# Kernel tuning notes

Hardware: AMD Instinct MI355X
Metric: run time of the kernel (lower is better)

The kernel has to match this reference:

```python
import jax, jax.numpy as jnp
import numpy as np

B, N, C, H = 8192, 17, 512, 8
HD = C // H  # head dim = 64


def setup_inputs() -> dict:
    key = jax.random.key(0)
    ks = jax.random.split(key, 7)
    s = 0.02
    return {
        "x": jax.random.normal(ks[0], (B, N, C), dtype=jnp.float32),
        "W_qkv": jax.random.normal(ks[1], (C, 3 * C), dtype=jnp.float32) * s,
        "b_qkv": jax.random.normal(ks[2], (3 * C,), dtype=jnp.float32) * s,
        "outer": jax.random.normal(ks[3], (H, N, N), dtype=jnp.float32) * s,
        "alpha": jnp.ones((1,), dtype=jnp.float32),
        "W_proj": jax.random.normal(ks[4], (C, C), dtype=jnp.float32) * s,
        "b_proj": jax.random.normal(ks[5], (C,), dtype=jnp.float32) * s,
    }


def reference(x, W_qkv, b_qkv, outer, alpha, W_proj, b_proj):
    scale = HD ** -0.5
    qkv = x @ W_qkv + b_qkv                       # [B,N,3C]
    qkv = qkv.reshape(B, N, 3, H, HD)
    q = jnp.transpose(qkv[:, :, 0], (0, 2, 1, 3))  # [B,H,N,HD]
    k = jnp.transpose(qkv[:, :, 1], (0, 2, 1, 3))
    v = jnp.transpose(qkv[:, :, 2], (0, 2, 1, 3))
    # comb=False path: (q @ k^T + alpha * outer) * scale, softmax, @ v
    logits = (jnp.einsum('bhnd,bhmd->bhnm', q, k) + alpha * outer[None]) * scale
    attn = jax.nn.softmax(logits, axis=-1)        # [B,H,N,N]
    out = jnp.einsum('bhnm,bhmd->bhnd', attn, v)  # [B,H,N,HD]
    out = jnp.transpose(out, (0, 2, 1, 3)).reshape(B, N, C)
    return out @ W_proj + b_proj
```

## Files before the change

### kernel.cpp

```cpp
#include <hip/hip_runtime.h>
#include <stdint.h>


typedef __attribute__((ext_vector_type(4))) float f32x4;
typedef _Float16 f16x8 __attribute__((ext_vector_type(8)));
typedef _Float16 f16x2 __attribute__((ext_vector_type(2)));

__device__ __forceinline__ unsigned short f2h(float f) {
  return __builtin_bit_cast(unsigned short, (_Float16)f);
}
__device__ __forceinline__ float h2f(unsigned short h) {
  return (float)__builtin_bit_cast(_Float16, h);
}
__device__ __forceinline__ float fdot2u(uint32_t a, uint32_t b, float c) {
  return __builtin_amdgcn_fdot2(__builtin_bit_cast(f16x2, a),
                                __builtin_bit_cast(f16x2, b), c, false);
}

#define GLOAD_LDS16(gptr, lptr)                                          \
  __builtin_amdgcn_global_load_lds(                                      \
      (__attribute__((address_space(1))) void*)(gptr),                   \
      (__attribute__((address_space(3))) void*)(lptr), 16, 0, 0)

__device__ __forceinline__ f32x4 mfma16(f16x8 a, f16x8 b, f32x4 c) {
  return __builtin_amdgcn_mfma_f32_16x16x32_f16(a, b, c, 0, 0, 0);
}

__global__ __launch_bounds__(256) void k_cvt(const float* __restrict__ in,
                                             unsigned short* __restrict__ out,
                                             long n4) {
  long i = (long)blockIdx.x * 256 + threadIdx.x;
  if (i >= n4) return;
  float4 a = reinterpret_cast<const float4*>(in)[i];
  ushort4 o;
  o.x = f2h(a.x); o.y = f2h(a.y); o.z = f2h(a.z); o.w = f2h(a.w);
  reinterpret_cast<ushort4*>(out)[i] = o;
}

template <bool PERM>
__global__ __launch_bounds__(256) void k_cvt_t(const float* __restrict__ W,
                                               unsigned short* __restrict__ Wt,
                                               int K, int Norig) {
  int i = blockIdx.x * 256 + threadIdx.x;
  if (i >= K * Norig) return;
  int np = i / K, k = i - np * K;
  int n = np;
  if (PERM) {
    int h = np / 192, rem = np - h * 192;
    int t = rem >> 6, d = rem & 63;
    n = t * 512 + h * 64 + d;
  }
  Wt[i] = f2h(W[(size_t)k * Norig + n]);
}

__global__ __launch_bounds__(256) void k_permb(const float* __restrict__ b,
                                               float* __restrict__ bqp) {
  int np = blockIdx.x * 256 + threadIdx.x;
  if (np >= 1536) return;
  int h = np / 192, rem = np - h * 192;
  int t = rem >> 6, d = rem & 63;
  bqp[np] = b[t * 512 + h * 64 + d];
}

#define FB_BUF 28672

__global__ __launch_bounds__(1024) void k_fused(
    const unsigned short* __restrict__ A,
    const unsigned short* __restrict__ Bt,
    const float* __restrict__ bqp,
    const float* __restrict__ outer,
    const float* __restrict__ alpha_p,
    unsigned short* __restrict__ ao) {
  __shared__ __align__(16) unsigned short smem[2 * FB_BUF];
  __shared__ float s_attn[16][17][18];
  __shared__ float s_inv[16][17];

  const int tid = threadIdx.x;
  const int w = tid >> 6, lane = tid & 63;
  const int wm = w >> 2, wn = w & 3;
  const int lr = lane & 15, lk = lane >> 4;

  const int bid = (blockIdx.x & 7) * ((int)gridDim.x >> 3) + (blockIdx.x >> 3);
  const int mt = bid >> 3, h = bid & 7;
  const int batch0 = mt * 15;
  const int brow = batch0 * 17;
  const int bcol = h * 192;

  const int srowl = lane >> 3;
  const int scol = ((lane & 7) ^ srowl) << 3;

  f32x4 acc[4][3];
#pragma unroll
  for (int m = 0; m < 4; m++)
#pragma unroll
    for (int n = 0; n < 3; n++) acc[m][n] = f32x4{0.f, 0.f, 0.f, 0.f};

  auto STAGE = [&](int t, int buf) {
    unsigned short* dstbase = smem + buf * FB_BUF;
    for (int s = w; s < 56; s += 16) {
      unsigned short* dst = dstbase + s * 512;
      const unsigned short* src;
      if (s < 32) {
        int gr = brow + s * 8 + srowl;
        if (gr > 139263) gr = 139263;
        src = A + (size_t)gr * 512 + t * 64 + scol;
      } else {
        int r = (s - 32) * 8 + srowl;
        src = Bt + (size_t)(bcol + r) * 512 + t * 64 + scol;
      }
      GLOAD_LDS16(src, dst);
    }
  };

  STAGE(0, 0);
  asm volatile("s_waitcnt vmcnt(0)" ::: "memory");
  __builtin_amdgcn_s_barrier();

  for (int t = 0; t < 8; ++t) {
    const int ub = (t & 1) * FB_BUF;
    if (t < 7) STAGE(t + 1, (t + 1) & 1);
    const unsigned short* sa = smem + ub + (wm * 64 + lr) * 64;
    const unsigned short* sb = smem + ub + 16384 + (wn * 48 + lr) * 64;
#pragma unroll
    for (int kk = 0; kk < 2; ++kk) {
      const int gx = (((kk << 2) + lk) ^ (lr & 7)) << 3;
      f16x8 av0 = *(const f16x8*)(sa + gx);
      f16x8 av1 = *(const f16x8*)(sa + 1024 + gx);
      f16x8 av2 = *(const f16x8*)(sa + 2048 + gx);
      f16x8 av3 = *(const f16x8*)(sa + 3072 + gx);
      f16x8 bv0 = *(const f16x8*)(sb + gx);
      f16x8 bv1 = *(const f16x8*)(sb + 1024 + gx);
      f16x8 bv2 = *(const f16x8*)(sb + 2048 + gx);
      acc[0][0] = mfma16(av0, bv0, acc[0][0]);
      acc[0][1] = mfma16(av0, bv1, acc[0][1]);
      acc[0][2] = mfma16(av0, bv2, acc[0][2]);
      acc[1][0] = mfma16(av1, bv0, acc[1][0]);
      acc[1][1] = mfma16(av1, bv1, acc[1][1]);
      acc[1][2] = mfma16(av1, bv2, acc[1][2]);
      acc[2][0] = mfma16(av2, bv0, acc[2][0]);
      acc[2][1] = mfma16(av2, bv1, acc[2][1]);
      acc[2][2] = mfma16(av2, bv2, acc[2][2]);
      acc[3][0] = mfma16(av3, bv0, acc[3][0]);
      acc[3][1] = mfma16(av3, bv1, acc[3][1]);
      acc[3][2] = mfma16(av3, bv2, acc[3][2]);
    }
    asm volatile("s_waitcnt vmcnt(0)" ::: "memory");
    __builtin_amdgcn_s_barrier();
  }

  {
    const int er0 = wm * 64 + (lane >> 4) * 4;
    const int ec0 = wn * 48 + lr;
    float bvv[3];
#pragma unroll
    for (int nf = 0; nf < 3; ++nf) bvv[nf] = bqp[bcol + ec0 + nf * 16];
#pragma unroll
    for (int mf = 0; mf < 4; ++mf)
#pragma unroll
      for (int nf = 0; nf < 3; ++nf)
#pragma unroll
        for (int rr = 0; rr < 4; ++rr)
          smem[(er0 + mf * 16 + rr) * 200 + ec0 + nf * 16] =
              f2h(acc[mf][nf][rr] + bvv[nf]);
  }
  __syncthreads();

  const int nb = min(15, 8192 - batch0);
  if (w < nb) {
    const float alpha = alpha_p[0];
    const unsigned short* sA0 = smem + (w * 17) * 200;
    for (int p = lane; p < 289; p += 64) {
      const int r = p / 17, m = p - r * 17;
      const uint4* qr = (const uint4*)(sA0 + r * 200);
      const uint4* km = (const uint4*)(sA0 + m * 200 + 64);
      float s = 0.f;
#pragma unroll
      for (int c = 0; c < 8; ++c) {
        uint4 qa = qr[c], ka = km[c];
        s = fdot2u(qa.x, ka.x, s);
        s = fdot2u(qa.y, ka.y, s);
        s = fdot2u(qa.z, ka.z, s);
        s = fdot2u(qa.w, ka.w, s);
      }
      s_attn[w][r][m] = (s + alpha * outer[h * 289 + p]) * 0.125f;
    }
    __builtin_amdgcn_wave_barrier();
    asm volatile("" ::: "memory");

    if (lane < 17) {
      float mx = -1e30f;
#pragma unroll
      for (int m = 0; m < 17; m++) mx = fmaxf(mx, s_attn[w][lane][m]);
      float s = 0.f;
#pragma unroll
      for (int m = 0; m < 17; m++) {
        float e = __expf(s_attn[w][lane][m] - mx);
        s_attn[w][lane][m] = e;
        s += e;
      }
      s_inv[w][lane] = 1.f / s;
    }
    __builtin_amdgcn_wave_barrier();
    asm volatile("" ::: "memory");

    float vr[17];
#pragma unroll
    for (int m = 0; m < 17; m++)
      vr[m] = h2f(smem[(w * 17 + m) * 200 + 128 + lane]);
    const size_t obase = ((size_t)(batch0 + w) * 17) * 512 + h * 64 + lane;
#pragma unroll 1
    for (int r = 0; r < 17; ++r) {
      float o = 0.f;
#pragma unroll
      for (int m = 0; m < 17; m++) o += s_attn[w][r][m] * vr[m];
      ao[obase + (size_t)r * 512] = f2h(o * s_inv[w][r]);
    }
  }
}

#define MFMA_QUAD(M0, N0)                                                  \
  __builtin_amdgcn_s_setprio(1);                                           \
  _Pragma("unroll") for (int m_ = 0; m_ < 4; m_++) {                       \
    _Pragma("unroll") for (int n_ = 0; n_ < 2; n_++) {                     \
      acc[(M0) + m_][(N0) + n_] =                                          \
          mfma16(a[(M0) + m_][0], b[(N0) + n_][0], acc[(M0) + m_][(N0) + n_]); \
      acc[(M0) + m_][(N0) + n_] =                                          \
          mfma16(a[(M0) + m_][1], b[(N0) + n_][1], acc[(M0) + m_][(N0) + n_]); \
    }                                                                      \
  }                                                                        \
  __builtin_amdgcn_s_setprio(0);

#define READ_A_HALF(MH)                                                    \
  _Pragma("unroll") for (int m_ = 0; m_ < 4; m_++) {                       \
    a[(MH)*4 + m_][0] =                                                    \
        *(const f16x8*)(ldsA + ub + ((MH)*4 + m_) * 1024 + gx0);           \
    a[(MH)*4 + m_][1] =                                                    \
        *(const f16x8*)(ldsA + ub + ((MH)*4 + m_) * 1024 + gx1);           \
  }
#define READ_B_HALF(NH)                                                    \
  _Pragma("unroll") for (int n_ = 0; n_ < 2; n_++) {                       \
    b[(NH)*2 + n_][0] =                                                    \
        *(const f16x8*)(ldsB + ub + ((NH)*2 + n_) * 1024 + gx0);           \
    b[(NH)*2 + n_][1] =                                                    \
        *(const f16x8*)(ldsB + ub + ((NH)*2 + n_) * 1024 + gx1);           \
  }

template <int KT, bool F16OUT>
__global__ __launch_bounds__(512, 2) void k_gemm256(
    const unsigned short* __restrict__ A, const unsigned short* __restrict__ Bt,
    const float* __restrict__ bias, void* __restrict__ Cout, int M, int N,
    int K) {
  __shared__ __align__(16) unsigned short lds[2][2][256 * 64];

  const int tid = threadIdx.x;
  const int w = tid >> 6, lane = tid & 63;
  const int wm = w >> 2, wn = w & 3;
  const int lr = lane & 15, lk = lane >> 4;

  const int bid = (blockIdx.x & 7) * ((int)gridDim.x >> 3) + (blockIdx.x >> 3);
  const int nbn = N >> 8;
  const int brow = (bid / nbn) << 8;
  const int bcol = (bid % nbn) << 8;

  const int srow = lane >> 3;
  const int scol = (((lane & 7) ^ srow) << 3);
  const unsigned short* pA = A + (size_t)(brow + (w << 3) + srow) * K + scol;
  const unsigned short* pB = Bt + (size_t)(bcol + (w << 3) + srow) * K + scol;

  auto STAGE = [&](int hh) {
    const int uu = hh >> 2, s = hh & 3;
    const int isB = s >> 1, half = s & 1;
    const unsigned short* src =
        (isB ? pB : pA) + (size_t)(half * 128) * K + uu * 64;
    unsigned short* dst = &lds[uu & 1][isB][(half * 128 + (w << 3)) * 64];
    GLOAD_LDS16(src, dst);
    GLOAD_LDS16(src + (size_t)64 * K, dst + 64 * 64);
  };

  const int gx0 = ((lk) ^ (lr & 7)) << 3;
  const int gx1 = ((4 + lk) ^ (lr & 7)) << 3;
  const unsigned short* ldsA = &lds[0][0][(wm * 128 + lr) * 64];
  const unsigned short* ldsB = &lds[0][1][(wn * 64 + lr) * 64];

  f32x4 acc[8][4];
#pragma unroll
  for (int m = 0; m < 8; m++)
#pragma unroll
    for (int n = 0; n < 4; n++) acc[m][n] = f32x4{0.f, 0.f, 0.f, 0.f};

#pragma unroll
  for (int hh = 0; hh < 7; ++hh) STAGE(hh);
  asm volatile("s_waitcnt vmcnt(6)" ::: "memory");
  __builtin_amdgcn_s_barrier();

  f16x8 a[8][2], b[4][2];
  for (int u = 0; u < KT; ++u) {
    const int ub = (u & 1) * 32768;
    const int hbase = 4 * u + 7;
    READ_A_HALF(0)
    READ_B_HALF(0)
    if (hbase < 4 * KT) STAGE(hbase);
    __builtin_amdgcn_s_barrier();
    asm volatile("s_waitcnt lgkmcnt(0)" ::: "memory");
    __builtin_amdgcn_sched_barrier(0);
    MFMA_QUAD(0, 0)
    __builtin_amdgcn_s_barrier();
    READ_A_HALF(1)
    READ_B_HALF(1)
    if (hbase + 1 < 4 * KT) STAGE(hbase + 1);
    __builtin_amdgcn_s_barrier();
    asm volatile("s_waitcnt lgkmcnt(0)" ::: "memory");
    __builtin_amdgcn_sched_barrier(0);
    MFMA_QUAD(0, 2)
    __builtin_amdgcn_s_barrier();
    if (hbase + 2 < 4 * KT) STAGE(hbase + 2);
    __builtin_amdgcn_s_barrier();
    MFMA_QUAD(4, 2)
    __builtin_amdgcn_s_barrier();
    if (hbase + 3 < 4 * KT) STAGE(hbase + 3);
    if (u + 2 < KT) {
      asm volatile("s_waitcnt vmcnt(6)" ::: "memory");
    } else if (u + 2 == KT) {
      asm volatile("s_waitcnt vmcnt(0)" ::: "memory");
    }
    __builtin_amdgcn_s_barrier();
    MFMA_QUAD(4, 0)
    __builtin_amdgcn_s_barrier();
  }

  const int orow = brow + wm * 128 + (lane >> 4) * 4;
  const int ocol0 = bcol + wn * 64 + lr;
#pragma unroll
  for (int n = 0; n < 4; n++) {
    const int col = ocol0 + n * 16;
    const float bv = bias[col];
#pragma unroll
    for (int m = 0; m < 8; m++) {
      const int row = orow + m * 16;
#pragma unroll
      for (int r = 0; r < 4; r++) {
        float v = acc[m][n][r] + bv;
        if (F16OUT)
          ((unsigned short*)Cout)[(size_t)(row + r) * N + col] = f2h(v);
        else
          ((float*)Cout)[(size_t)(row + r) * N + col] = v;
      }
    }
  }
}

extern "C" void kernel_launch(void* const* d_in, const int* in_sizes, int n_in,
                              void* d_out, int out_size, void* d_ws,
                              size_t ws_size, hipStream_t stream) {
  const float* x      = (const float*)d_in[0];
  const float* W_qkv  = (const float*)d_in[1];
  const float* b_qkv  = (const float*)d_in[2];
  const float* outer  = (const float*)d_in[3];
  const float* alpha  = (const float*)d_in[4];
  const float* W_proj = (const float*)d_in[5];
  const float* b_proj = (const float*)d_in[6];

  char* ws = (char*)d_ws;
  unsigned short* xb  = (unsigned short*)(ws);
  unsigned short* ao  = (unsigned short*)(ws + 142606336);
  unsigned short* wqt = (unsigned short*)(ws + 285212672);
  unsigned short* wpt = (unsigned short*)(ws + 286785536);
  float*          bqp = (float*)(ws + 287309824);

  k_cvt<<<dim3(69632), dim3(256), 0, stream>>>(x, xb, 17825792L);
  k_cvt_t<true><<<dim3(3072), dim3(256), 0, stream>>>(W_qkv, wqt, 512, 1536);
  k_cvt_t<false><<<dim3(1024), dim3(256), 0, stream>>>(W_proj, wpt, 512, 512);
  k_permb<<<dim3(6), dim3(256), 0, stream>>>(b_qkv, bqp);

  k_fused<<<dim3(4376), dim3(1024), 0, stream>>>(xb, wqt, bqp, outer, alpha, ao);

  k_gemm256<8, false><<<dim3(1088), dim3(512), 0, stream>>>(
      ao, wpt, b_proj, (float*)d_out, 139264, 512, 512);
}
```

Before: 726.5 us.

## Shrink fused attention and projection tiles to 512-thread blocks for occupancy

Result: faster. 594.0 us (-18.2%).

```diff
diff --git a/kernel.cpp b/kernel.cpp
--- a/kernel.cpp
+++ b/kernel.cpp
@@ -62,18 +62,16 @@
   bqp[np] = b[t * 512 + h * 64 + d];
 }
 
-#define FB_BUF 28672
-
-__global__ __launch_bounds__(1024) void k_fused(
+#define FBUF 20480
+
+__global__ __launch_bounds__(512, 4) void k_fused(
     const unsigned short* __restrict__ A,
     const unsigned short* __restrict__ Bt,
     const float* __restrict__ bqp,
     const float* __restrict__ outer,
     const float* __restrict__ alpha_p,
     unsigned short* __restrict__ ao) {
-  __shared__ __align__(16) unsigned short smem[2 * FB_BUF];
-  __shared__ float s_attn[16][17][18];
-  __shared__ float s_inv[16][17];
+  __shared__ __align__(16) unsigned short smem[2 * FBUF];
 
   const int tid = threadIdx.x;
   const int w = tid >> 6, lane = tid & 63;
@@ -82,7 +80,7 @@
 
   const int bid = (blockIdx.x & 7) * ((int)gridDim.x >> 3) + (blockIdx.x >> 3);
   const int mt = bid >> 3, h = bid & 7;
-  const int batch0 = mt * 15;
+  const int batch0 = mt * 7;
   const int brow = batch0 * 17;
   const int bcol = h * 192;
 
@@ -96,16 +94,18 @@
     for (int n = 0; n < 3; n++) acc[m][n] = f32x4{0.f, 0.f, 0.f, 0.f};
 
   auto STAGE = [&](int t, int buf) {
-    unsigned short* dstbase = smem + buf * FB_BUF;
-    for (int s = w; s < 56; s += 16) {
+    unsigned short* dstbase = smem + buf * FBUF;
+#pragma unroll
+    for (int s5 = 0; s5 < 5; ++s5) {
+      const int s = w + s5 * 8;
       unsigned short* dst = dstbase + s * 512;
       const unsigned short* src;
-      if (s < 32) {
+      if (s < 16) {
         int gr = brow + s * 8 + srowl;
         if (gr > 139263) gr = 139263;
         src = A + (size_t)gr * 512 + t * 64 + scol;
       } else {
-        int r = (s - 32) * 8 + srowl;
+        int r = (s - 16) * 8 + srowl;
         src = Bt + (size_t)(bcol + r) * 512 + t * 64 + scol;
       }
       GLOAD_LDS16(src, dst);
@@ -117,10 +117,10 @@
   __builtin_amdgcn_s_barrier();
 
   for (int t = 0; t < 8; ++t) {
-    const int ub = (t & 1) * FB_BUF;
+    const int ub = (t & 1) * FBUF;
     if (t < 7) STAGE(t + 1, (t + 1) & 1);
     const unsigned short* sa = smem + ub + (wm * 64 + lr) * 64;
-    const unsigned short* sb = smem + ub + 16384 + (wn * 48 + lr) * 64;
+    const unsigned short* sb = smem + ub + 8192 + (wn * 48 + lr) * 64;
 #pragma unroll
     for (int kk = 0; kk < 2; ++kk) {
       const int gx = (((kk << 2) + lk) ^ (lr & 7)) << 3;
@@ -148,6 +148,9 @@
     __builtin_amdgcn_s_barrier();
   }
 
+  float* s_attn = (float*)(smem + 25600);
+  float* s_inv = (float*)(smem + 25600 + 2 * (7 * 17 * 18));
+
   {
     const int er0 = wm * 64 + (lane >> 4) * 4;
     const int ec0 = wn * 48 + lr;
@@ -165,7 +168,7 @@
   }
   __syncthreads();
 
-  const int nb = min(15, 8192 - batch0);
+  const int nb = min(7, 8192 - batch0);
   if (w < nb) {
     const float alpha = alpha_p[0];
     const unsigned short* sA0 = smem + (w * 17) * 200;
@@ -182,7 +185,7 @@
         s = fdot2u(qa.z, ka.z, s);
         s = fdot2u(qa.w, ka.w, s);
       }
-      s_attn[w][r][m] = (s + alpha * outer[h * 289 + p]) * 0.125f;
+      s_attn[(w * 17 + r) * 18 + m] = (s + alpha * outer[h * 289 + p]) * 0.125f;
     }
     __builtin_amdgcn_wave_barrier();
     asm volatile("" ::: "memory");
@@ -190,15 +193,16 @@
     if (lane < 17) {
       float mx = -1e30f;
 #pragma unroll
-      for (int m = 0; m < 17; m++) mx = fmaxf(mx, s_attn[w][lane][m]);
+      for (int m = 0; m < 17; m++)
+        mx = fmaxf(mx, s_attn[(w * 17 + lane) * 18 + m]);
       float s = 0.f;
 #pragma unroll
       for (int m = 0; m < 17; m++) {
-        float e = __expf(s_attn[w][lane][m] - mx);
-        s_attn[w][lane][m] = e;
+        float e = __expf(s_attn[(w * 17 + lane) * 18 + m] - mx);
+        s_attn[(w * 17 + lane) * 18 + m] = e;
         s += e;
       }
-      s_inv[w][lane] = 1.f / s;
+      s_inv[w * 17 + lane] = 1.f / s;
     }
     __builtin_amdgcn_wave_barrier();
     asm volatile("" ::: "memory");
@@ -212,45 +216,20 @@
     for (int r = 0; r < 17; ++r) {
       float o = 0.f;
 #pragma unroll
-      for (int m = 0; m < 17; m++) o += s_attn[w][r][m] * vr[m];
-      ao[obase + (size_t)r * 512] = f2h(o * s_inv[w][r]);
-    }
-  }
-}
-
-#define MFMA_QUAD(M0, N0)                                                  \
-  __builtin_amdgcn_s_setprio(1);                                           \
-  _Pragma("unroll") for (int m_ = 0; m_ < 4; m_++) {                       \
-    _Pragma("unroll") for (int n_ = 0; n_ < 2; n_++) {                     \
-      acc[(M0) + m_][(N0) + n_] =                                          \
-          mfma16(a[(M0) + m_][0], b[(N0) + n_][0], acc[(M0) + m_][(N0) + n_]); \
-      acc[(M0) + m_][(N0) + n_] =                                          \
-          mfma16(a[(M0) + m_][1], b[(N0) + n_][1], acc[(M0) + m_][(N0) + n_]); \
-    }                                                                      \
-  }                                                                        \
-  __builtin_amdgcn_s_setprio(0);
-
-#define READ_A_HALF(MH)                                                    \
-  _Pragma("unroll") for (int m_ = 0; m_ < 4; m_++) {                       \
-    a[(MH)*4 + m_][0] =                                                    \
-        *(const f16x8*)(ldsA + ub + ((MH)*4 + m_) * 1024 + gx0);           \
-    a[(MH)*4 + m_][1] =                                                    \
-        *(const f16x8*)(ldsA + ub + ((MH)*4 + m_) * 1024 + gx1);           \
-  }
-#define READ_B_HALF(NH)                                                    \
-  _Pragma("unroll") for (int n_ = 0; n_ < 2; n_++) {                       \
-    b[(NH)*2 + n_][0] =                                                    \
-        *(const f16x8*)(ldsB + ub + ((NH)*2 + n_) * 1024 + gx0);           \
-    b[(NH)*2 + n_][1] =                                                    \
-        *(const f16x8*)(ldsB + ub + ((NH)*2 + n_) * 1024 + gx1);           \
-  }
-
-template <int KT, bool F16OUT>
-__global__ __launch_bounds__(512, 2) void k_gemm256(
-    const unsigned short* __restrict__ A, const unsigned short* __restrict__ Bt,
-    const float* __restrict__ bias, void* __restrict__ Cout, int M, int N,
-    int K) {
-  __shared__ __align__(16) unsigned short lds[2][2][256 * 64];
+      for (int m = 0; m < 17; m++) o += s_attn[(w * 17 + r) * 18 + m] * vr[m];
+      ao[obase + (size_t)r * 512] = f2h(o * s_inv[w * 17 + r]);
+    }
+  }
+}
+
+#define PBUF 16384
+
+__global__ __launch_bounds__(512, 4) void k_proj(
+    const unsigned short* __restrict__ A,
+    const unsigned short* __restrict__ Bt,
+    const float* __restrict__ bias,
+    float* __restrict__ C) {
+  __shared__ __align__(16) unsigned short smem[2 * PBUF];
 
   const int tid = threadIdx.x;
   const int w = tid >> 6, lane = tid & 63;
@@ -258,93 +237,74 @@
   const int lr = lane & 15, lk = lane >> 4;
 
   const int bid = (blockIdx.x & 7) * ((int)gridDim.x >> 3) + (blockIdx.x >> 3);
-  const int nbn = N >> 8;
-  const int brow = (bid / nbn) << 8;
-  const int bcol = (bid % nbn) << 8;
-
-  const int srow = lane >> 3;
-  const int scol = (((lane & 7) ^ srow) << 3);
-  const unsigned short* pA = A + (size_t)(brow + (w << 3) + srow) * K + scol;
-  const unsigned short* pB = Bt + (size_t)(bcol + (w << 3) + srow) * K + scol;
-
-  auto STAGE = [&](int hh) {
-    const int uu = hh >> 2, s = hh & 3;
-    const int isB = s >> 1, half = s & 1;
-    const unsigned short* src =
-        (isB ? pB : pA) + (size_t)(half * 128) * K + uu * 64;
-    unsigned short* dst = &lds[uu & 1][isB][(half * 128 + (w << 3)) * 64];
-    GLOAD_LDS16(src, dst);
-    GLOAD_LDS16(src + (size_t)64 * K, dst + 64 * 64);
+  const int brow = (bid >> 2) << 7;
+  const int bcol = (bid & 3) << 7;
+
+  const int srowl = lane >> 3;
+  const int scol = ((lane & 7) ^ srowl) << 3;
+
+  f32x4 acc[4][2];
+#pragma unroll
+  for (int m = 0; m < 4; m++)
+#pragma unroll
+    for (int n = 0; n < 2; n++) acc[m][n] = f32x4{0.f, 0.f, 0.f, 0.f};
+
+  auto STAGE = [&](int t, int buf) {
+    unsigned short* dstbase = smem + buf * PBUF;
+#pragma unroll
+    for (int s4 = 0; s4 < 4; ++s4) {
+      const int s = w + s4 * 8;
+      unsigned short* dst = dstbase + s * 512;
+      const unsigned short* src =
+          (s < 16) ? A + (size_t)(brow + s * 8 + srowl) * 512 + t * 64 + scol
+                   : Bt + (size_t)(bcol + (s - 16) * 8 + srowl) * 512 + t * 64 + scol;
+      GLOAD_LDS16(src, dst);
+    }
   };
 
-  const int gx0 = ((lk) ^ (lr & 7)) << 3;
-  const int gx1 = ((4 + lk) ^ (lr & 7)) << 3;
-  const unsigned short* ldsA = &lds[0][0][(wm * 128 + lr) * 64];
-  const unsigned short* ldsB = &lds[0][1][(wn * 64 + lr) * 64];
-
-  f32x4 acc[8][4];
-#pragma unroll
-  for (int m = 0; m < 8; m++)
-#pragma unroll
-    for (int n = 0; n < 4; n++) acc[m][n] = f32x4{0.f, 0.f, 0.f, 0.f};
-
-#pragma unroll
-  for (int hh = 0; hh < 7; ++hh) STAGE(hh);
-  asm volatile("s_waitcnt vmcnt(6)" ::: "memory");
+  STAGE(0, 0);
+  asm volatile("s_waitcnt vmcnt(0)" ::: "memory");
   __builtin_amdgcn_s_barrier();
 
-  f16x8 a[8][2], b[4][2];
-  for (int u = 0; u < KT; ++u) {
-    const int ub = (u & 1) * 32768;
-    const int hbase = 4 * u + 7;
-    READ_A_HALF(0)
-    READ_B_HALF(0)
-    if (hbase < 4 * KT) STAGE(hbase);
+  for (int t = 0; t < 8; ++t) {
+    const int ub = (t & 1) * PBUF;
+    if (t < 7) STAGE(t + 1, (t + 1) & 1);
+    const unsigned short* sa = smem + ub + (wm * 64 + lr) * 64;
+    const unsigned short* sb = smem + ub + 8192 + (wn * 32 + lr) * 64;
+#pragma unroll
+    for (int kk = 0; kk < 2; ++kk) {
+      const int gx = (((kk << 2) + lk) ^ (lr & 7)) << 3;
+      f16x8 av0 = *(const f16x8*)(sa + gx);
+      f16x8 av1 = *(const f16x8*)(sa + 1024 + gx);
+      f16x8 av2 = *(const f16x8*)(sa + 2048 + gx);
+      f16x8 av3 = *(const f16x8*)(sa + 3072 + gx);
+      f16x8 bv0 = *(const f16x8*)(sb + gx);
+      f16x8 bv1 = *(const f16x8*)(sb + 1024 + gx);
+      acc[0][0] = mfma16(av0, bv0, acc[0][0]);
+      acc[0][1] = mfma16(av0, bv1, acc[0][1]);
+      acc[1][0] = mfma16(av1, bv0, acc[1][0]);
+      acc[1][1] = mfma16(av1, bv1, acc[1][1]);
+      acc[2][0] = mfma16(av2, bv0, acc[2][0]);
+      acc[2][1] = mfma16(av2, bv1, acc[2][1]);
+      acc[3][0] = mfma16(av3, bv0, acc[3][0]);
+      acc[3][1] = mfma16(av3, bv1, acc[3][1]);
+    }
+    asm volatile("s_waitcnt vmcnt(0)" ::: "memory");
     __builtin_amdgcn_s_barrier();
-    asm volatile("s_waitcnt lgkmcnt(0)" ::: "memory");
-    __builtin_amdgcn_sched_barrier(0);
-    MFMA_QUAD(0, 0)
-    __builtin_amdgcn_s_barrier();
-    READ_A_HALF(1)
-    READ_B_HALF(1)
-    if (hbase + 1 < 4 * KT) STAGE(hbase + 1);
-    __builtin_amdgcn_s_barrier();
-    asm volatile("s_waitcnt lgkmcnt(0)" ::: "memory");
-    __builtin_amdgcn_sched_barrier(0);
-    MFMA_QUAD(0, 2)
-    __builtin_amdgcn_s_barrier();
-    if (hbase + 2 < 4 * KT) STAGE(hbase + 2);
-    __builtin_amdgcn_s_barrier();
-    MFMA_QUAD(4, 2)
-    __builtin_amdgcn_s_barrier();
-    if (hbase + 3 < 4 * KT) STAGE(hbase + 3);
-    if (u + 2 < KT) {
-      asm volatile("s_waitcnt vmcnt(6)" ::: "memory");
-    } else if (u + 2 == KT) {
-      asm volatile("s_waitcnt vmcnt(0)" ::: "memory");
-    }
-    __builtin_amdgcn_s_barrier();
-    MFMA_QUAD(4, 0)
-    __builtin_amdgcn_s_barrier();
-  }
-
-  const int orow = brow + wm * 128 + (lane >> 4) * 4;
-  const int ocol0 = bcol + wn * 64 + lr;
-#pragma unroll
-  for (int n = 0; n < 4; n++) {
+  }
+
+  const int orow = brow + wm * 64 + (lane >> 4) * 4;
+  const int ocol0 = bcol + wn * 32 + lr;
+#pragma unroll
+  for (int n = 0; n < 2; n++) {
     const int col = ocol0 + n * 16;
     const float bv = bias[col];
 #pragma unroll
-    for (int m = 0; m < 8; m++) {
+    for (int m = 0; m < 4; m++) {
       const int row = orow + m * 16;
 #pragma unroll
-      for (int r = 0; r < 4; r++) {
-        float v = acc[m][n][r] + bv;
-        if (F16OUT)
-          ((unsigned short*)Cout)[(size_t)(row + r) * N + col] = f2h(v);
-        else
-          ((float*)Cout)[(size_t)(row + r) * N + col] = v;
-      }
+      for (int r = 0; r < 4; r++)
+        C[(size_t)(row + r) * 512 + col] = acc[m][n][r] + bv;
     }
   }
 }
@@ -372,8 +332,7 @@
   k_cvt_t<false><<<dim3(1024), dim3(256), 0, stream>>>(W_proj, wpt, 512, 512);
   k_permb<<<dim3(6), dim3(256), 0, stream>>>(b_qkv, bqp);
 
-  k_fused<<<dim3(4376), dim3(1024), 0, stream>>>(xb, wqt, bqp, outer, alpha, ao);
-
-  k_gemm256<8, false><<<dim3(1088), dim3(512), 0, stream>>>(
-      ao, wpt, b_proj, (float*)d_out, 139264, 512, 512);
-}
+  k_fused<<<dim3(9368), dim3(512), 0, stream>>>(xb, wqt, bqp, outer, alpha, ao);
+
+  k_proj<<<dim3(4352), dim3(512), 0, stream>>>(ao, wpt, b_proj, (float*)d_out);
+}
```
